# Performance work log

Hardware: AMD Instinct MI355X
Metric: run time of the kernel (lower is better)

The kernel has to match this reference:

```python
import itertools
import jax, jax.numpy as jnp
import numpy as np

B, N, C, O = 8, 32, 64, 64
PERMS = list(itertools.permutations((1, 2, 3)))  # build_idx_3_permutations order


def _lin(k, fan_in, out, lead=()):
    # torch nn.Linear default init: U(-1/sqrt(fan_in), 1/sqrt(fan_in)) for W and b
    kw, kb = jax.random.split(k)
    bound = 1.0 / float(np.sqrt(fan_in))
    W = jax.random.uniform(kw, lead + (fan_in, out), minval=-bound, maxval=bound, dtype=jnp.float32)
    b = jax.random.uniform(kb, lead + (out,), minval=-bound, maxval=bound, dtype=jnp.float32)
    return W, b


def setup_inputs() -> dict:
    key = jax.random.key(0)
    ks = jax.random.split(key, 8)
    x = jax.random.normal(ks[0], (B, N, N, N, C), dtype=jnp.float32)
    W33, b33 = _lin(ks[1], 6 * C, O)            # three_to_three linear
    W22, b22 = _lin(ks[2], 12 * C, O, (3,))     # two_to_two (a2 cat transpose), 3 diagonal planes
    W12, b12 = _lin(ks[3], 10 * C, O, (3,))     # one_to_two
    W12t, b12t = _lin(ks[4], 10 * C, O, (3,))   # one_to_two_t
    W02, b02 = _lin(ks[5], 5 * C, O, (3,))      # zero_to_two
    W11, b11 = _lin(ks[6], 10 * C, O)           # one_to_one (in_node_channels = 0)
    W01, b01 = _lin(ks[7], 5 * C, O)            # zero_to_one
    return dict(x=x, W33=W33, b33=b33, W22=W22, b22=b22, W12=W12, b12=b12,
                W12t=W12t, b12t=b12t, W02=W02, b02=b02, W11=W11, b11=b11,
                W01=W01, b01=b01)


def _contractions(x):
    """All second/first/zeroth-order mean contractions of x: [B,n,n,n,C]."""
    s1, s2, s3 = x.mean(1), x.mean(2), x.mean(3)                      # [B,n,n,C]
    # diagonals arranged as [B, other_axis, diag_axis, C]
    d12 = jnp.moveaxis(jnp.diagonal(x, axis1=1, axis2=2), -1, 2)      # [B,n3,diag,C]
    d13 = jnp.moveaxis(jnp.diagonal(x, axis1=1, axis2=3), -1, 2)      # [B,n2,diag,C]
    d23 = jnp.moveaxis(jnp.diagonal(x, axis1=2, axis2=3), -1, 2)      # [B,n1,diag,C]
    a2 = jnp.concatenate([s1, s2, s3, d12, d13, d23], axis=-1)        # [B,n,n,6C]
    tdiag = jnp.moveaxis(jnp.diagonal(d23, axis1=1, axis2=2), -1, 1)  # [B,n,C] triple diagonal x[b,i,i,i]
    a1 = jnp.concatenate([
        x.mean((1, 2)), x.mean((1, 3)), x.mean((2, 3)),               # double sums
        d12.mean(1), d12.mean(2), d13.mean(1), d13.mean(2),           # diag sums
        d23.mean(1), d23.mean(2),
        tdiag], axis=-1)                                              # [B,n,10C]
    a0 = jnp.concatenate([
        x.mean((1, 2, 3)),                                            # triple sum
        d12.mean((1, 2)), d13.mean((1, 2)), d23.mean((1, 2)),         # diag-sum-sum
        tdiag.mean(1)], axis=-1)                                      # [B,5C]
    return a2, a1, a0


def reference(x, W33, b33, W22, b22, W12, b12, W12t, b12t, W02, b02, W11, b11, W01, b01):
    n = x.shape[1]
    a2, a1, a0 = _contractions(x)
    # third-order mix: concat all 6 spatial permutations, then linear 6C -> O
    allp = jnp.concatenate([jnp.transpose(x, (0,) + p + (4,)) for p in PERMS], axis=-1)
    T = allp @ W33 + b33                                              # [B,n,n,n,O]
    # second-order mixes for the 3 diagonal planes
    a2wt = jnp.concatenate([a2, jnp.swapaxes(a2, 1, 2)], axis=-1)     # [B,n,n,12C]
    slices = []
    for i in range(3):
        m = a2wt @ W22[i] + b22[i]
        m = m + (a1 @ W12[i] + b12[i])[:, :, None, :]
        m = m + (a1 @ W12t[i] + b12t[i])[:, None, :, :]
        m = m + (a0 @ W02[i] + b02[i])[:, None, None, :]
        slices.append(m)                                              # [B,n(other),n(diag),O]
    # first-order (core-diagonal) mix
    mdiag = a1 @ W11 + b11 + (a0 @ W01 + b01)[:, None, :]             # [B,n,O]
    # _expand_mix: accumulate slices onto diagonal planes of T (diagonal_free=False)
    idx = jnp.arange(n)
    # plane (1,2): T[b,d,d,t] += slices[0][b,t,d]
    T = T.at[:, idx, idx].add(jnp.swapaxes(slices[0], 1, 2))
    # plane (1,3): T[b,d,t,d] += slices[1][b,t,d]
    Tsw = jnp.swapaxes(T, 2, 3)
    Tsw = Tsw.at[:, idx, idx].add(jnp.swapaxes(slices[1], 1, 2))
    T = jnp.swapaxes(Tsw, 2, 3)
    # plane (2,3): T[b,t,d,d] += slices[2][b,t,d]
    T = T.at[:, :, idx, idx].add(slices[2])
    # triple diagonal: T[b,d,d,d] += mdiag[b,d]
    T = T.at[:, idx, idx, idx].add(mdiag)
    return T
```

## Files before the change

kernel.cpp:

```cpp
#include <hip/hip_runtime.h>

#define NBATCH 8
#define NN 32
#define NC 64
#define NO 64
#define C6 384
#define C10 640
#define C12 768
#define C5 320

typedef __attribute__((ext_vector_type(8))) short short8;
typedef __attribute__((ext_vector_type(4))) float float4v;

static constexpr int OFF_ABF = 0;
static constexpr int OFF_A1  = 1572864;
static constexpr int OFF_A0  = 1736704;
static constexpr int OFF_R1  = 1739264;
static constexpr int OFF_R1T = 1788416;
static constexpr int OFF_R0  = 1837568;
static constexpr int OFF_MD  = 1839104;
static constexpr int OFF_WB  = 1855488;
static constexpr int OFF_WB2 = 1867776;

__device__ __forceinline__ unsigned short f2bf(float f) {
    union { float f; unsigned u; } x{f};
    unsigned r = x.u + 0x7fffu + ((x.u >> 16) & 1u);
    return (unsigned short)(r >> 16);
}

__device__ __forceinline__ void store_bf4(unsigned short* p, float4v v) {
    ushort4 w;
    w.x = f2bf(v.x); w.y = f2bf(v.y); w.z = f2bf(v.z); w.w = f2bf(v.w);
    *(ushort4*)p = w;
}

__device__ __forceinline__ float4v bf4(const unsigned short* p) {
    ushort4 u = *(const ushort4*)(p);
    float4v r;
    r.x = __uint_as_float((unsigned)u.x << 16);
    r.y = __uint_as_float((unsigned)u.y << 16);
    r.z = __uint_as_float((unsigned)u.z << 16);
    r.w = __uint_as_float((unsigned)u.w << 16);
    return r;
}

__global__ __launch_bounds__(256) void k_prep2(const float* __restrict__ W33,
                                               const float* __restrict__ W22,
                                               const float* __restrict__ x,
                                               float* __restrict__ ws) {
    if (blockIdx.x < 84) {
        int id = blockIdx.x * 256 + threadIdx.x;
        if (id < 3072) {
            int lane = id & 63;
            int ks = (id >> 6) % 12;
            int nt = (id >> 6) / 12;
            int n = nt * 16 + (lane & 15);
            int k0 = ks * 32 + (lane >> 4) * 8;
            unsigned short* dst = (unsigned short*)(ws + OFF_WB) +
                                  (size_t)((nt * 12 + ks) * 64 + lane) * 8;
#pragma unroll
            for (int jj = 0; jj < 8; ++jj) dst[jj] = f2bf(W33[(k0 + jj) * 64 + n]);
        } else if (id < 21504) {
            int q = id - 3072;
            int lane = q & 63;
            int ks = (q >> 6) % 24;
            int r = (q >> 6) / 24;
            int nt = r & 3;
            int i = r >> 2;
            int n = nt * 16 + (lane & 15);
            int k0 = ks * 32 + (lane >> 4) * 8;
            const float* W = W22 + (size_t)i * C12 * NO;
            unsigned short* dst = (unsigned short*)(ws + OFF_WB2) +
                                  (size_t)(((i * 4 + nt) * 24 + ks) * 64 + lane) * 8;
#pragma unroll
            for (int jj = 0; jj < 8; ++jj) dst[jj] = f2bf(W[(k0 + jj) * 64 + n]);
        }
        return;
    }
    int qb = blockIdx.x - 84;
    int cls = qb >> 9;
    int id = (qb & 511) * 256 + threadIdx.x;
    int c4 = id & 15;
    int v = (id >> 4) & 31;
    int u = (id >> 9) & 31;
    int b = id >> 14;
    int bc = c4 * 4;
    const float* xb = x + (size_t)b * 2097152;
    unsigned short* a2 = (unsigned short*)(ws + OFF_ABF) +
                         (size_t)((b * 32 + u) * 32 + v) * C6 + bc;
    const float inv = 1.0f / 32.0f;
    float4v s = {0.f, 0.f, 0.f, 0.f};

    if (cls == 0) {
        const float* p = xb + u * 2048 + v * 64 + bc;
        for (int i = 0; i < 32; ++i) s += *(const float4v*)(p + i * 65536);
        float4v d12 = *(const float4v*)(xb + v * 65536 + v * 2048 + u * 64 + bc);
        store_bf4(a2 + 0 * 64, s * inv);
        store_bf4(a2 + 3 * 64, d12);
    } else if (cls == 1) {
        const float* p = xb + u * 65536 + v * 64 + bc;
        for (int j = 0; j < 32; ++j) s += *(const float4v*)(p + j * 2048);
        float4v d13 = *(const float4v*)(xb + v * 65536 + u * 2048 + v * 64 + bc);
        store_bf4(a2 + 1 * 64, s * inv);
        store_bf4(a2 + 4 * 64, d13);
    } else {
        const float* p = xb + u * 65536 + v * 2048 + bc;
        for (int k = 0; k < 32; ++k) s += *(const float4v*)(p + k * 64);
        float4v d23 = *(const float4v*)(xb + u * 65536 + v * 2048 + v * 64 + bc);
        store_bf4(a2 + 2 * 64, s * inv);
        store_bf4(a2 + 5 * 64, d23);
    }
}

__global__ __launch_bounds__(256) void k_contract1(const float* __restrict__ x,
                                                   float* __restrict__ ws) {
    __shared__ float4v red[16][148];
    int blk = blockIdx.x;
    int b = blk >> 5;
    int t = blk & 31;
    int tid = threadIdx.x;
    int c4 = tid & 15;
    int q = tid >> 4;
    int bc = c4 * 4;
    const unsigned short* a2 = (const unsigned short*)(ws + OFF_ABF) +
                               (size_t)b * 32 * 32 * C6;

    float4v pu0 = {0.f, 0.f, 0.f, 0.f};
    float4v pu3 = pu0, pu4 = pu0, pu5 = pu0;
    float4v pv0 = pu0, pv1 = pu0, pv3 = pu0, pv4 = pu0, pv5 = pu0;
#pragma unroll
    for (int s = 0; s < 2; ++s) {
        int u = q * 2 + s;
        const unsigned short* rU = a2 + (size_t)(u * 32 + t) * C6 + bc;
        const unsigned short* rV = a2 + (size_t)(t * 32 + u) * C6 + bc;
        pu0 += bf4(rU + 0);
        pu3 += bf4(rU + 192);
        pu4 += bf4(rU + 256);
        pu5 += bf4(rU + 320);
        pv0 += bf4(rV + 0);
        pv1 += bf4(rV + 64);
        pv3 += bf4(rV + 192);
        pv4 += bf4(rV + 256);
        pv5 += bf4(rV + 320);
    }
    red[q][0 * 16 + c4] = pu0;
    red[q][1 * 16 + c4] = pv0;
    red[q][2 * 16 + c4] = pv1;
    red[q][3 * 16 + c4] = pu3;
    red[q][4 * 16 + c4] = pv3;
    red[q][5 * 16 + c4] = pu4;
    red[q][6 * 16 + c4] = pv4;
    red[q][7 * 16 + c4] = pu5;
    red[q][8 * 16 + c4] = pv5;
    __syncthreads();

    const float inv = 1.0f / 32.0f;
    float* a1 = ws + OFF_A1 + ((size_t)b * 32 + t) * C10;
    float* a0 = ws + OFF_A0 + (size_t)b * C5;
    if (tid < 144) {
        int ch = tid >> 4;
        int cc = tid & 15;
        float4v s = {0.f, 0.f, 0.f, 0.f};
#pragma unroll
        for (int qq = 0; qq < 16; ++qq) s += red[qq][ch * 16 + cc];
        s *= inv;
        *(float4v*)(a1 + ch * 64 + cc * 4) = s;
        int aidx = (ch == 0) ? 0 : (ch == 3) ? 1 : (ch == 5) ? 2 : (ch == 7) ? 3 : -1;
        if (aidx >= 0) {
#pragma unroll
            for (int e = 0; e < 4; ++e)
                atomicAdd(a0 + aidx * 64 + cc * 4 + e, s[e] * inv);
        }
    } else if (tid < 160) {
        int cc = tid - 144;
        float4v td = *(const float4v*)(x + (((size_t)b * 32 + t) * 32 + t) * 2048 +
                                       t * 64 + cc * 4);
        *(float4v*)(a1 + 9 * 64 + cc * 4) = td;
#pragma unroll
        for (int e = 0; e < 4; ++e)
            atomicAdd(a0 + 4 * 64 + cc * 4 + e, td[e] * inv);
    }
}

__global__ __launch_bounds__(256) void k_mainmix(
    const float* __restrict__ x, const float* __restrict__ ws_c,
    const float* __restrict__ b33, float* __restrict__ T,
    const float* __restrict__ W12, const float* __restrict__ b12,
    const float* __restrict__ W12t, const float* __restrict__ b12t,
    const float* __restrict__ W02, const float* __restrict__ b02,
    const float* __restrict__ W11, const float* __restrict__ b11,
    const float* __restrict__ W01, const float* __restrict__ b01,
    float* __restrict__ ws) {
    __shared__ __align__(16) unsigned short As[32 * 392];
    int tid = threadIdx.x;

    if (blockIdx.x < 454) {
        int id = blockIdx.x * 256 + tid;
        if (id < 98304) {
            bool second = id >= 49152;
            int q = second ? id - 49152 : id;
            int o = q & 63;
            int t = (q >> 6) & 31;
            int b = (q >> 11) & 7;
            int i = q >> 14;
            const float* W = (second ? W12t : W12) + (size_t)i * C10 * NO;
            const float* bb = (second ? b12t : b12) + i * NO;
            const float* a1 = ws + OFF_A1 + ((size_t)b * 32 + t) * C10;
            float acc = bb[o];
            for (int m = 0; m < C10; ++m) acc += a1[m] * W[m * NO + o];
            ws[(second ? OFF_R1T : OFF_R1) + (((size_t)i * 8 + b) * 32 + t) * NO + o] = acc;
        } else if (id < 114688) {
            int q = id - 98304;
            int o = q & 63;
            int t = (q >> 6) & 31;
            int b = q >> 11;
            const float* a1 = ws + OFF_A1 + ((size_t)b * 32 + t) * C10;
            const float* a0 = ws + OFF_A0 + (size_t)b * C5;
            float acc = b11[o] + b01[o];
            for (int m = 0; m < C10; ++m) acc += a1[m] * W11[m * NO + o];
            for (int m = 0; m < C5; ++m) acc += a0[m] * W01[m * NO + o];
            ws[OFF_MD + ((size_t)b * 32 + t) * NO + o] = acc;
        } else if (id < 116224) {
            int q = id - 114688;
            int o = q & 63;
            int b = (q >> 6) & 7;
            int i = q >> 9;
            const float* a0 = ws + OFF_A0 + (size_t)b * C5;
            float acc = b02[i * NO + o];
            for (int m = 0; m < C5; ++m) acc += a0[m] * W02[(size_t)i * C5 * NO + m * NO + o];
            ws[OFF_R0 + ((size_t)i * 8 + b) * NO + o] = acc;
        }
        return;
    }

    const unsigned short* WB = (const unsigned short*)(ws_c + OFF_WB);

    int wv = tid >> 6;
    int lane = tid & 63;
    int m_tile = wv & 1;
    int n_pair = wv >> 1;
    int colq = lane & 15;
    int quad = lane >> 4;

    short8 bfr[2][12];
#pragma unroll
    for (int np = 0; np < 2; ++np) {
        int nt = n_pair * 2 + np;
#pragma unroll
        for (int ks = 0; ks < 12; ++ks)
            bfr[np][ks] = *(const short8*)(WB + (size_t)((nt * 12 + ks) * 64 + lane) * 8);
    }
    float bb0 = b33[(n_pair * 2 + 0) * 16 + colq];
    float bb1 = b33[(n_pair * 2 + 1) * 16 + colq];

    int k0 = wv * 8;
    int c = colq * 4;
    int mrow = m_tile * 16 + colq;
    const unsigned short* Arow = &As[mrow * 392 + quad * 8];

    int q = blockIdx.x - 454;
    int tbase = (q & 7) * 1024 + (q >> 3) * 4;
#pragma unroll 1
    for (int r = 0; r < 4; ++r) {
        int tile = tbase + r;
        int b = tile >> 10;
        int i = (tile >> 5) & 31;
        int j = tile & 31;
        const float* xb = x + (size_t)b * 2097152;

#pragma unroll
        for (int half = 0; half < 2; ++half) {
            int k = k0 + quad + half * 4;
            float4v v0 = *(const float4v*)(xb + i * 65536 + j * 2048 + k * 64 + c);
            float4v v1 = *(const float4v*)(xb + i * 65536 + k * 2048 + j * 64 + c);
            float4v v2 = *(const float4v*)(xb + j * 65536 + i * 2048 + k * 64 + c);
            float4v v3 = *(const float4v*)(xb + k * 65536 + i * 2048 + j * 64 + c);
            float4v v4 = *(const float4v*)(xb + j * 65536 + k * 2048 + i * 64 + c);
            float4v v5 = *(const float4v*)(xb + k * 65536 + j * 2048 + i * 64 + c);
            unsigned short* dst = &As[k * 392 + c];
            store_bf4(dst + 0 * 64, v0);
            store_bf4(dst + 1 * 64, v1);
            store_bf4(dst + 2 * 64, v2);
            store_bf4(dst + 3 * 64, v3);
            store_bf4(dst + 4 * 64, v4);
            store_bf4(dst + 5 * 64, v5);
        }
        __syncthreads();

        float4v acc0 = {0.f, 0.f, 0.f, 0.f};
        float4v acc1 = {0.f, 0.f, 0.f, 0.f};
#pragma unroll
        for (int ks = 0; ks < 12; ++ks) {
            short8 a = *(const short8*)(Arow + ks * 32);
            acc0 = __builtin_amdgcn_mfma_f32_16x16x32_bf16(a, bfr[0][ks], acc0, 0, 0, 0);
            acc1 = __builtin_amdgcn_mfma_f32_16x16x32_bf16(a, bfr[1][ks], acc1, 0, 0, 0);
        }

        float* Tb = T + (size_t)tile * 2048;
#pragma unroll
        for (int rr = 0; rr < 4; ++rr) {
            int m = m_tile * 16 + quad * 4 + rr;
            int o0 = (n_pair * 2 + 0) * 16 + colq;
            int o1 = (n_pair * 2 + 1) * 16 + colq;
            __builtin_nontemporal_store(acc0[rr] + bb0, &Tb[m * 64 + o0]);
            __builtin_nontemporal_store(acc1[rr] + bb1, &Tb[m * 64 + o1]);
        }
        __syncthreads();
    }
}

__global__ __launch_bounds__(256) void k_slices(const float* __restrict__ b22,
                                                float* __restrict__ T,
                                                const float* __restrict__ ws) {
    __shared__ __align__(16) unsigned short As[32 * 776];
    int blk = blockIdx.x;
    int i = blk >> 8;
    int bt = blk & 255;
    int b = bt >> 5;
    int t = bt & 31;
    int tid = threadIdx.x;
    const unsigned short* abf = (const unsigned short*)(ws + OFF_ABF);
    const unsigned short* WB2 = (const unsigned short*)(ws + OFF_WB2);

    for (int l = tid; l < 3072; l += 256) {
        int d = l / 96;
        int m8 = l - d * 96;
        const unsigned short* src = (m8 < 48)
            ? abf + (size_t)(((b * 32 + t) * 32 + d) * C6) + m8 * 8
            : abf + (size_t)(((b * 32 + d) * 32 + t) * C6) + (m8 - 48) * 8;
        *(short8*)&As[d * 776 + m8 * 8] = *(const short8*)src;
    }
    __syncthreads();

    int wv = tid >> 6;
    int lane = tid & 63;
    int mt = wv & 1;
    int nh = wv >> 1;
    float4v zero = {0.f, 0.f, 0.f, 0.f};
    float4v acc[2] = {zero, zero};
    const unsigned short* Arow = &As[(mt * 16 + (lane & 15)) * 776 + (lane >> 4) * 8];
#pragma unroll
    for (int ks = 0; ks < 24; ++ks) {
        short8 a = *(const short8*)(Arow + ks * 32);
#pragma unroll
        for (int np = 0; np < 2; ++np) {
            int nt = nh * 2 + np;
            short8 bf = *(const short8*)(WB2 + (size_t)(((i * 4 + nt) * 24 + ks) * 64 + lane) * 8);
            acc[np] = __builtin_amdgcn_mfma_f32_16x16x32_bf16(a, bf, acc[np], 0, 0, 0);
        }
    }

    int colq = lane & 15;
    int quad = lane >> 4;
    float* Tb = T + (size_t)b * 2097152;
#pragma unroll
    for (int np = 0; np < 2; ++np) {
        int o = (nh * 2 + np) * 16 + colq;
        float base = b22[i * 64 + o] + ws[OFF_R1 + (((size_t)i * 8 + b) * 32 + t) * 64 + o]
                   + ws[OFF_R0 + ((size_t)i * 8 + b) * 64 + o];
#pragma unroll
        for (int r = 0; r < 4; ++r) {
            int d = mt * 16 + quad * 4 + r;
            float s = acc[np][r] + base +
                      ws[OFF_R1T + (((size_t)i * 8 + b) * 32 + d) * 64 + o];
            if (d != t) {
                size_t addr = (i == 0) ? (size_t)d * 65536 + d * 2048 + t * 64 + o
                            : (i == 1) ? (size_t)d * 65536 + t * 2048 + d * 64 + o
                                       : (size_t)t * 65536 + d * 2048 + d * 64 + o;
                Tb[addr] += s;
            } else {
                if (i == 0) s += ws[OFF_MD + ((size_t)b * 32 + d) * 64 + o];
                atomicAdd(&Tb[(size_t)d * 65536 + d * 2048 + d * 64 + o], s);
            }
        }
    }
}

extern "C" void kernel_launch(void* const* d_in, const int* in_sizes, int n_in,
                              void* d_out, int out_size, void* d_ws, size_t ws_size,
                              hipStream_t stream) {
    const float* x    = (const float*)d_in[0];
    const float* W33  = (const float*)d_in[1];
    const float* b33  = (const float*)d_in[2];
    const float* W22  = (const float*)d_in[3];
    const float* b22  = (const float*)d_in[4];
    const float* W12  = (const float*)d_in[5];
    const float* b12  = (const float*)d_in[6];
    const float* W12t = (const float*)d_in[7];
    const float* b12t = (const float*)d_in[8];
    const float* W02  = (const float*)d_in[9];
    const float* b02  = (const float*)d_in[10];
    const float* W11  = (const float*)d_in[11];
    const float* b11  = (const float*)d_in[12];
    const float* W01  = (const float*)d_in[13];
    const float* b01  = (const float*)d_in[14];
    float* T  = (float*)d_out;
    float* ws = (float*)d_ws;

    hipMemsetAsync(ws + OFF_A0, 0, (size_t)NBATCH * C5 * sizeof(float), stream);
    hipLaunchKernelGGL(k_prep2, dim3(1620), dim3(256), 0, stream, W33, W22, x, ws);
    hipLaunchKernelGGL(k_contract1, dim3(256), dim3(256), 0, stream, x, ws);
    hipLaunchKernelGGL(k_mainmix, dim3(2502), dim3(256), 0, stream,
                       x, ws, b33, T, W12, b12, W12t, b12t, W02, b02,
                       W11, b11, W01, b01, ws);
    hipLaunchKernelGGL(k_slices, dim3(768), dim3(256), 0, stream, b22, T, ws);
}
```

Before: 237.5 us.

## Move slice GEMMs into mainmix kernel and add a lightweight scatter epilogue

The diagonal-plane slice GEMMs are split into two K-halves (a2 and its transpose) and computed as extra blocks of the main mix kernel, so they overlap with the big three-to-three GEMM. Results go to a workspace buffer. A new elementwise epilogue kernel sums the halves and the broadcast terms, then scatters all three planes in one pass without atomics. The cost is an extra workspace round trip of the slice outputs and more blocks in the main kernel. It also relies on the slice blocks' LDS (the As array) being large enough for the smaller 392-stride tile.

```diff
diff --git a/kernel.cpp b/kernel.cpp
--- a/kernel.cpp
+++ b/kernel.cpp
@@ -21,6 +21,7 @@
 static constexpr int OFF_MD  = 1839104;
 static constexpr int OFF_WB  = 1855488;
 static constexpr int OFF_WB2 = 1867776;
+static constexpr int OFF_SLC = 1941504;
 
 __device__ __forceinline__ unsigned short f2bf(float f) {
     union { float f; unsigned u; } x{f};
@@ -233,6 +234,63 @@
         return;
     }
 
+    if (blockIdx.x >= 2502) {
+        int q2 = blockIdx.x - 2502;
+        int bt = q2 & 255;
+        int r6 = q2 >> 8;
+        int i = r6 % 3;
+        int h = r6 / 3;
+        int b = bt >> 5;
+        int t = bt & 31;
+        const unsigned short* abf = (const unsigned short*)(ws_c + OFF_ABF);
+        const unsigned short* WB2 = (const unsigned short*)(ws_c + OFF_WB2);
+
+        for (int l = tid; l < 1536; l += 256) {
+            int d = l / 48;
+            int m8 = l - d * 48;
+            int r0 = h ? d : t;
+            int r1 = h ? t : d;
+            const unsigned short* src =
+                abf + (size_t)(((b * 32 + r0) * 32 + r1) * C6) + m8 * 8;
+            *(short8*)&As[d * 392 + m8 * 8] = *(const short8*)src;
+        }
+        __syncthreads();
+
+        int wv = tid >> 6;
+        int lane = tid & 63;
+        int mt = wv & 1;
+        int nh = wv >> 1;
+        float4v zero = {0.f, 0.f, 0.f, 0.f};
+        float4v acc[2] = {zero, zero};
+        const unsigned short* Arow = &As[(mt * 16 + (lane & 15)) * 392 + (lane >> 4) * 8];
+#pragma unroll
+        for (int ks = 0; ks < 12; ++ks) {
+            short8 a = *(const short8*)(Arow + ks * 32);
+#pragma unroll
+            for (int np = 0; np < 2; ++np) {
+                int nt = nh * 2 + np;
+                short8 bf = *(const short8*)(WB2 +
+                    (size_t)(((i * 4 + nt) * 24 + (h * 12 + ks)) * 64 + lane) * 8);
+                acc[np] = __builtin_amdgcn_mfma_f32_16x16x32_bf16(a, bf, acc[np], 0, 0, 0);
+            }
+        }
+
+        int colq = lane & 15;
+        int quad = lane >> 4;
+        float* slc = ws + OFF_SLC +
+                     ((((size_t)(h * 3 + i) * 8 + b) * 32 + t) * 32) * 64;
+#pragma unroll
+        for (int np = 0; np < 2; ++np) {
+            int o = (nh * 2 + np) * 16 + colq;
+#pragma unroll
+            for (int rr = 0; rr < 4; ++rr) {
+                int d = mt * 16 + quad * 4 + rr;
+                slc[d * 64 + o] = acc[np][rr];
+            }
+        }
+        return;
+    }
+
     const unsigned short* WB = (const unsigned short*)(ws_c + OFF_WB);
 
     int wv = tid >> 6;
@@ -309,70 +367,34 @@
     }
 }
 
-__global__ __launch_bounds__(256) void k_slices(const float* __restrict__ b22,
-                                                float* __restrict__ T,
-                                                const float* __restrict__ ws) {
-    __shared__ __align__(16) unsigned short As[32 * 776];
-    int blk = blockIdx.x;
-    int i = blk >> 8;
-    int bt = blk & 255;
-    int b = bt >> 5;
-    int t = bt & 31;
-    int tid = threadIdx.x;
-    const unsigned short* abf = (const unsigned short*)(ws + OFF_ABF);
-    const unsigned short* WB2 = (const unsigned short*)(ws + OFF_WB2);
-
-    for (int l = tid; l < 3072; l += 256) {
-        int d = l / 96;
-        int m8 = l - d * 96;
-        const unsigned short* src = (m8 < 48)
-            ? abf + (size_t)(((b * 32 + t) * 32 + d) * C6) + m8 * 8
-            : abf + (size_t)(((b * 32 + d) * 32 + t) * C6) + (m8 - 48) * 8;
-        *(short8*)&As[d * 776 + m8 * 8] = *(const short8*)src;
-    }
-    __syncthreads();
-
-    int wv = tid >> 6;
-    int lane = tid & 63;
-    int mt = wv & 1;
-    int nh = wv >> 1;
-    float4v zero = {0.f, 0.f, 0.f, 0.f};
-    float4v acc[2] = {zero, zero};
-    const unsigned short* Arow = &As[(mt * 16 + (lane & 15)) * 776 + (lane >> 4) * 8];
-#pragma unroll
-    for (int ks = 0; ks < 24; ++ks) {
-        short8 a = *(const short8*)(Arow + ks * 32);
-#pragma unroll
-        for (int np = 0; np < 2; ++np) {
-            int nt = nh * 2 + np;
-            short8 bf = *(const short8*)(WB2 + (size_t)(((i * 4 + nt) * 24 + ks) * 64 + lane) * 8);
-            acc[np] = __builtin_amdgcn_mfma_f32_16x16x32_bf16(a, bf, acc[np], 0, 0, 0);
-        }
-    }
-
-    int colq = lane & 15;
-    int quad = lane >> 4;
+__global__ __launch_bounds__(256) void k_slices_ep(const float* __restrict__ b22,
+                                                   float* __restrict__ T,
+                                                   const float* __restrict__ ws) {
+    int id = blockIdx.x * 256 + threadIdx.x;
+    int o = id & 63;
+    int d = (id >> 6) & 31;
+    int t = (id >> 11) & 31;
+    int b = id >> 16;
+    const float* slc0 = ws + OFF_SLC;
+    const float* slc1 = ws + OFF_SLC + 3 * 8 * 32 * 32 * 64;
+
+    float s[3];
+#pragma unroll
+    for (int i = 0; i < 3; ++i) {
+        size_t idx = ((((size_t)i * 8 + b) * 32 + t) * 32 + d) * 64 + o;
+        s[i] = slc0[idx] + slc1[idx] + b22[i * 64 + o]
+             + ws[OFF_R1 + (((size_t)i * 8 + b) * 32 + t) * 64 + o]
+             + ws[OFF_R0 + ((size_t)i * 8 + b) * 64 + o]
+             + ws[OFF_R1T + (((size_t)i * 8 + b) * 32 + d) * 64 + o];
+    }
     float* Tb = T + (size_t)b * 2097152;
-#pragma unroll
-    for (int np = 0; np < 2; ++np) {
-        int o = (nh * 2 + np) * 16 + colq;
-        float base = b22[i * 64 + o] + ws[OFF_R1 + (((size_t)i * 8 + b) * 32 + t) * 64 + o]
-                   + ws[OFF_R0 + ((size_t)i * 8 + b) * 64 + o];
-#pragma unroll
-        for (int r = 0; r < 4; ++r) {
-            int d = mt * 16 + quad * 4 + r;
-            float s = acc[np][r] + base +
-                      ws[OFF_R1T + (((size_t)i * 8 + b) * 32 + d) * 64 + o];
-            if (d != t) {
-                size_t addr = (i == 0) ? (size_t)d * 65536 + d * 2048 + t * 64 + o
-                            : (i == 1) ? (size_t)d * 65536 + t * 2048 + d * 64 + o
-                                       : (size_t)t * 65536 + d * 2048 + d * 64 + o;
-                Tb[addr] += s;
-            } else {
-                if (i == 0) s += ws[OFF_MD + ((size_t)b * 32 + d) * 64 + o];
-                atomicAdd(&Tb[(size_t)d * 65536 + d * 2048 + d * 64 + o], s);
-            }
-        }
+    if (d != t) {
+        Tb[d * 65536 + d * 2048 + t * 64 + o] += s[0];
+        Tb[d * 65536 + t * 2048 + d * 64 + o] += s[1];
+        Tb[t * 65536 + d * 2048 + d * 64 + o] += s[2];
+    } else {
+        Tb[d * 65536 + d * 2048 + d * 64 + o] +=
+            s[0] + s[1] + s[2] + ws[OFF_MD + ((size_t)b * 32 + d) * 64 + o];
     }
 }
 
@@ -400,8 +422,8 @@
     hipMemsetAsync(ws + OFF_A0, 0, (size_t)NBATCH * C5 * sizeof(float), stream);
     hipLaunchKernelGGL(k_prep2, dim3(1620), dim3(256), 0, stream, W33, W22, x, ws);
     hipLaunchKernelGGL(k_contract1, dim3(256), dim3(256), 0, stream, x, ws);
-    hipLaunchKernelGGL(k_mainmix, dim3(2502), dim3(256), 0, stream,
+    hipLaunchKernelGGL(k_mainmix, dim3(4038), dim3(256), 0, stream,
                        x, ws, b33, T, W12, b12, W12t, b12t, W02, b02,
                        W11, b11, W01, b01, ws);
-    hipLaunchKernelGGL(k_slices, dim3(768), dim3(256), 0, stream, b22, T, ws);
-}
+    hipLaunchKernelGGL(k_slices_ep, dim3(2048), dim3(256), 0, stream, b22, T, ws);
+}
```

Measured after the change: 238.3 us. About the same (+0.3%).
